# Optimization experiments

Measured on AMD Instinct MI355X. Metric: run time of the kernel, lower is better.

Reference implementation:

```python
import jax, jax.numpy as jnp
import numpy as np

LN_EPS = 1e-5
BN_EPS = 1e-5
N_TARGETS = 7


def setup_inputs() -> dict:
    key = jax.random.key(0)
    ks = jax.random.split(key, 12)
    B, N, W, Fin = 64, 40, 256, 64
    H, D = 4, 32
    C = H * D  # gat_out = 128
    L, K = 4, 3  # tcn layers / kernel
    FC = 128
    x = jax.random.normal(ks[0], (B, N, W, Fin), dtype=jnp.float32)
    adj = (jax.random.uniform(ks[1], (N, N)) < 0.3).astype(jnp.float32)
    adj = jnp.maximum(adj, jnp.eye(N, dtype=jnp.float32))  # self-loops
    s = 0.05
    return {
        "x": x,
        "adj": adj,
        "gat_w": jax.random.normal(ks[2], (C, Fin), dtype=jnp.float32) * s,
        "a_src": jax.random.normal(ks[3], (H, D), dtype=jnp.float32) * s,
        "a_dst": jax.random.normal(ks[4], (H, D), dtype=jnp.float32) * s,
        "ln_g": jnp.ones((C,), jnp.float32),
        "ln_b": jnp.zeros((C,), jnp.float32),
        "c1w": jax.random.normal(ks[5], (L, C, C, K), dtype=jnp.float32) * s,
        "c1b": jnp.zeros((L, C), jnp.float32),
        "c2w": jax.random.normal(ks[6], (L, C, C, K), dtype=jnp.float32) * s,
        "c2b": jnp.zeros((L, C), jnp.float32),
        "bn1s": jnp.ones((L, C), jnp.float32),
        "bn1b": jnp.zeros((L, C), jnp.float32),
        "bn1m": jnp.zeros((L, C), jnp.float32),
        "bn1v": jnp.ones((L, C), jnp.float32),
        "bn2s": jnp.ones((L, C), jnp.float32),
        "bn2b": jnp.zeros((L, C), jnp.float32),
        "bn2m": jnp.zeros((L, C), jnp.float32),
        "bn2v": jnp.ones((L, C), jnp.float32),
        "f1w": jax.random.normal(ks[7], (FC, C), dtype=jnp.float32) * s,
        "f1b": jnp.zeros((FC,), jnp.float32),
        "f2w": jax.random.normal(ks[8], (1, FC), dtype=jnp.float32) * s,
        "f2b": jnp.zeros((1,), jnp.float32),
    }


def reference(x, adj, gat_w, a_src, a_dst, ln_g, ln_b,
              c1w, c1b, c2w, c2b,
              bn1s, bn1b, bn1m, bn1v, bn2s, bn2b, bn2m, bn2v,
              f1w, f1b, f2w, f2b):
    B, N, W, Fin = x.shape
    H, D = a_src.shape
    C = H * D
    # --- GAT, vectorized over all W timesteps at once (same math as the per-t loop) ---
    h = jnp.einsum('bnwf,of->bnwo', x, gat_w).reshape(B, N, W, H, D)
    e_src = jnp.einsum('bnwhd,hd->bnwh', h, a_src)  # (B,N,W,H)
    e_dst = jnp.einsum('bnwhd,hd->bnwh', h, a_dst)
    # scores[b,i,w,h,j] = leaky_relu(e_src[b,i] + e_dst[b,j])
    scores = e_src[:, :, :, :, None] + jnp.transpose(e_dst, (0, 2, 3, 1))[:, None]  # (B,N,W,H,N)
    scores = jax.nn.leaky_relu(scores, 0.2)
    mask = adj[None, :, None, None, :] != 0
    scores = jnp.where(mask, scores, -1e9)
    attn = jax.nn.softmax(scores, axis=-1)  # softmax over destination j
    gat = jnp.einsum('bnwhj,bjwhd->bnwhd', attn, h).reshape(B, N, W, C)
    # --- LayerNorm over feature dim ---
    mu = gat.mean(-1, keepdims=True)
    var = gat.var(-1, keepdims=True)
    g = (gat - mu) / jnp.sqrt(var + LN_EPS) * ln_g + ln_b
    # --- TCN over per-node temporal sequences: (B*N, C, W) ---
    seq = jnp.transpose(g.reshape(B * N, W, C), (0, 2, 1))
    K = c1w.shape[-1]

    def bn(z, s, b, m, v):
        return (z - m[None, :, None]) / jnp.sqrt(v[None, :, None] + BN_EPS) * s[None, :, None] + b[None, :, None]

    def cconv(z, w, b, dil):
        pad = (K - 1) * dil  # causal left-padding
        y = jax.lax.conv_general_dilated(z, w, window_strides=(1,), padding=[(pad, 0)],
                                         rhs_dilation=(dil,), dimension_numbers=('NCH', 'OIH', 'NCH'))
        return y + b[None, :, None]

    cur = seq
    for i in range(c1w.shape[0]):  # fixed small number of TCN blocks
        dil = 2 ** i
        o = jax.nn.gelu(bn(cconv(cur, c1w[i], c1b[i], dil), bn1s[i], bn1b[i], bn1m[i], bn1v[i]), approximate=False)
        o = jax.nn.gelu(bn(cconv(o, c2w[i], c2b[i], dil), bn2s[i], bn2b[i], bn2m[i], bn2v[i]), approximate=False)
        cur = jax.nn.gelu(o + cur, approximate=False)  # residual is Identity (in_ch == out_ch)
    h_last = cur[:, :, -1].reshape(B, N, C)
    t = h_last[:, :N_TARGETS, :]  # target_indices = range(7)
    z = jax.nn.gelu(jnp.einsum('bnc,hc->bnh', t, f1w) + f1b, approximate=False)
    logits = (jnp.einsum('bnh,oh->bno', z, f2w) + f2b)[..., 0]  # (B, 7)
    return logits
```

## Files before the change

kernel.cpp:

```cpp
#include <hip/hip_runtime.h>
#include <hip/hip_bf16.h>
#include <math.h>

#define Bb   64
#define Nn   40
#define Ww   256
#define FIN  64
#define Hh   4
#define Dd   32
#define Cc   128
#define NT   7
#define FC   128
#define WT   61
#define W0   195
#define PSTRIDE 520
#define HS   132

#define SEQHI_OFF  0u
#define SEQ_BYTES  (448u * WT * Cc * 2u)
#define SEQLO_OFF  (SEQHI_OFF + SEQ_BYTES)
#define WBH_OFF    (SEQLO_OFF + SEQ_BYTES)
#define WB_BYTES   (8u * 4u * 24u * 64u * 8u * 2u)
#define WBL_OFF    (WBH_OFF + WB_BYTES)
#define PSB_OFF    (WBL_OFF + WB_BYTES)
#define PSS_OFF    (PSB_OFF + 4096u)
#define PSH_OFF    (PSS_OFF + 4096u)
#define WGH_OFF    (PSH_OFF + 4096u)
#define WGL_OFF    (WGH_OFF + 16384u)
#define WPHASE_US  49152u

typedef __attribute__((ext_vector_type(8)))  short short8;
typedef __attribute__((ext_vector_type(16))) float f32x16;

__device__ __forceinline__ float gelu_exact(float v) {
    return 0.5f * v * (1.0f + erff(v * 0.70710678118654752440f));
}
__device__ __forceinline__ float b2f(ushort u) {
    union { uint i; float f; } c; c.i = ((uint)u) << 16; return c.f;
}
__device__ __forceinline__ void split_bf16(float v, ushort& h, ushort& l) {
    __hip_bfloat16 bh = __float2bfloat16(v);
    float fh = __bfloat162float(bh);
    __hip_bfloat16 bl = __float2bfloat16(v - fh);
    h = *(ushort*)&bh; l = *(ushort*)&bl;
}

__global__ __launch_bounds__(256) void prep_kernel(
    const float* __restrict__ c1w, const float* __restrict__ c1b,
    const float* __restrict__ c2w, const float* __restrict__ c2b,
    const float* __restrict__ bn1s, const float* __restrict__ bn1b,
    const float* __restrict__ bn1m, const float* __restrict__ bn1v,
    const float* __restrict__ bn2s, const float* __restrict__ bn2b,
    const float* __restrict__ bn2m, const float* __restrict__ bn2v,
    const float* __restrict__ gat_w,
    char* __restrict__ ws)
{
    if (blockIdx.x < 192) {
        const int t = blockIdx.x * 256 + threadIdx.x;
        const int lane  = t & 63;
        const int kstep = (t >> 6) % 24;
        const int nt    = ((t >> 6) / 24) & 3;
        const int p     = (t >> 6) / 96;
        const int l = p >> 1, cv = p & 1;
        const int co = nt * 32 + (lane & 31);
        const float* wsrc = cv ? c2w : c1w;
        ushort* wbh = (ushort*)(ws + WBH_OFF);
        ushort* wbl = (ushort*)(ws + WBL_OFF);
#pragma unroll
        for (int j = 0; j < 8; ++j) {
            const int k  = kstep * 16 + ((lane >> 5) << 3) + j;
            const int kk = k >> 7, ci = k & 127;
            const float w = wsrc[((size_t)(l * Cc + co) * Cc + ci) * 3 + kk];
            ushort h, lo; split_bf16(w, h, lo);
            wbh[(size_t)t * 8 + j] = h;
            wbl[(size_t)t * 8 + j] = lo;
        }
    } else if (blockIdx.x == 192) {
        float* psb = (float*)(ws + PSB_OFF);
        float* pss = (float*)(ws + PSS_OFF);
        float* psh = (float*)(ws + PSH_OFF);
        for (int idx = threadIdx.x; idx < 1024; idx += 256) {
            const int p = idx >> 7, co = idx & 127;
            const int l = p >> 1, cv = p & 1;
            const int lc = l * Cc + co;
            const float s  = cv ? bn2s[lc] : bn1s[lc];
            const float bb = cv ? bn2b[lc] : bn1b[lc];
            const float m  = cv ? bn2m[lc] : bn1m[lc];
            const float vv = cv ? bn2v[lc] : bn1v[lc];
            const float cb = cv ? c2b[lc] : c1b[lc];
            const float scale = s * rsqrtf(vv + 1e-5f);
            pss[idx] = scale;
            psh[idx] = bb - m * scale;
            psb[idx] = cb;
        }
    } else {
        ushort* wgh = (ushort*)(ws + WGH_OFF);
        ushort* wgl = (ushort*)(ws + WGL_OFF);
#pragma unroll
        for (int it = 0; it < 4; ++it) {
            const int t = it * 256 + threadIdx.x;
            const int lane = t & 63;
            const int ks   = (t >> 6) & 3;
            const int nt   = t >> 8;
            const int co   = nt * 32 + (lane & 31);
#pragma unroll
            for (int j = 0; j < 8; ++j) {
                const int k = ks * 16 + ((lane >> 5) << 3) + j;
                ushort h, lo; split_bf16(gat_w[co * FIN + k], h, lo);
                wgh[t * 8 + j] = h;
                wgl[t * 8 + j] = lo;
            }
        }
    }
}

__global__ __launch_bounds__(256) void gat_ln_kernel(
    const float* __restrict__ x, const float* __restrict__ adj,
    const char* __restrict__ ws_ro,
    const float* __restrict__ a_src, const float* __restrict__ a_dst,
    const float* __restrict__ ln_g, const float* __restrict__ ln_b,
    ushort* __restrict__ seq_hi, ushort* __restrict__ seq_lo)
{
    __shared__ __align__(16) ushort xa_hi[8 * PSTRIDE];
    __shared__ __align__(16) ushort xa_lo[8 * PSTRIDE];
    __shared__ __align__(16) float h_lds[Nn * HS];
    __shared__ __align__(16) float e_lds[2 * Nn * Hh];
    __shared__ __align__(16) float attn_lds[NT * Hh * Nn];
    __shared__ __align__(16) float g_lds[NT * Cc];

    const int tid = threadIdx.x;
    const int blk = blockIdx.x;
    const int b   = blk / WT;
    const int tau = blk % WT;
    const int w   = W0 + tau;

    for (int idx = tid; idx < Nn * 8; idx += 256) {
        const int n  = idx >> 3;
        const int oc = idx & 7;
        const float* src = x + ((size_t)(b * Nn + n) * Ww + w) * FIN + oc * 8;
        const float4 f0 = *(const float4*)(src);
        const float4 f1 = *(const float4*)(src + 4);
        ushort h[8], l[8];
        split_bf16(f0.x, h[0], l[0]); split_bf16(f0.y, h[1], l[1]);
        split_bf16(f0.z, h[2], l[2]); split_bf16(f0.w, h[3], l[3]);
        split_bf16(f1.x, h[4], l[4]); split_bf16(f1.y, h[5], l[5]);
        split_bf16(f1.z, h[6], l[6]); split_bf16(f1.w, h[7], l[7]);
        const int dst = oc * PSTRIDE + n * 8;
        *(uint4*)(xa_hi + dst) = *(uint4*)h;
        *(uint4*)(xa_lo + dst) = *(uint4*)l;
    }
    for (int idx = tid; idx < 8 * (64 - Nn); idx += 256) {
        const int oc = idx / (64 - Nn);
        const int n  = Nn + idx % (64 - Nn);
        const int dst = oc * PSTRIDE + n * 8;
        uint4 z; z.x = z.y = z.z = z.w = 0u;
        *(uint4*)(xa_hi + dst) = z;
        *(uint4*)(xa_lo + dst) = z;
    }
    __syncthreads();

    {
        const int wave = tid >> 6;
        const int lane = tid & 63;
        const int nt   = wave;
        const int q2   = lane >> 5;
        const int m32  = lane & 31;
        const ushort* WGH = (const ushort*)(ws_ro + WGH_OFF);
        const ushort* WGL = (const ushort*)(ws_ro + WGL_OFF);

        f32x16 acc0, acc1;
#pragma unroll
        for (int i = 0; i < 16; ++i) { acc0[i] = 0.f; acc1[i] = 0.f; }

#pragma unroll
        for (int ks = 0; ks < 4; ++ks) {
            const size_t wo = ((size_t)((nt * 4 + ks) * 64 + lane)) * 8;
            const short8 bh = *(const short8*)(WGH + wo);
            const short8 bl = *(const short8*)(WGL + wo);
            const int pan = (ks * 2 + q2) * PSTRIDE;
            const short8 ah0 = *(const short8*)(xa_hi + pan + m32 * 8);
            const short8 al0 = *(const short8*)(xa_lo + pan + m32 * 8);
            const short8 ah1 = *(const short8*)(xa_hi + pan + (32 + m32) * 8);
            const short8 al1 = *(const short8*)(xa_lo + pan + (32 + m32) * 8);
            acc0 = __builtin_amdgcn_mfma_f32_32x32x16_bf16(ah0, bh, acc0, 0, 0, 0);
            acc0 = __builtin_amdgcn_mfma_f32_32x32x16_bf16(al0, bh, acc0, 0, 0, 0);
            acc0 = __builtin_amdgcn_mfma_f32_32x32x16_bf16(ah0, bl, acc0, 0, 0, 0);
            acc1 = __builtin_amdgcn_mfma_f32_32x32x16_bf16(ah1, bh, acc1, 0, 0, 0);
            acc1 = __builtin_amdgcn_mfma_f32_32x32x16_bf16(al1, bh, acc1, 0, 0, 0);
            acc1 = __builtin_amdgcn_mfma_f32_32x32x16_bf16(ah1, bl, acc1, 0, 0, 0);
        }

        const int co = nt * 32 + m32;
#pragma unroll
        for (int reg = 0; reg < 16; ++reg) {
            const int n = (reg & 3) + 8 * (reg >> 2) + 4 * q2;
            h_lds[n * HS + co] = acc0[reg];
        }
#pragma unroll
        for (int reg = 0; reg < 4; ++reg) {
            const int n = 32 + reg + 4 * q2;
            if (n < Nn) h_lds[n * HS + co] = acc1[reg];
        }
    }
    __syncthreads();

    for (int u = tid; u < 2 * Nn * Hh; u += 256) {
        const int s  = u & 1;
        const int hh = (u >> 1) & 3;
        const int n  = u >> 3;
        const float* av = (s ? a_dst : a_src) + hh * Dd;
        const float* hp = h_lds + n * HS + hh * Dd;
        float acc = 0.f;
#pragma unroll
        for (int i = 0; i < 8; ++i) {
            const float4 hv = *(const float4*)(hp + i * 4);
            const float4 avv = *(const float4*)(av + i * 4);
            acc += hv.x * avv.x + hv.y * avv.y + hv.z * avv.z + hv.w * avv.w;
        }
        e_lds[s * (Nn * Hh) + n * Hh + hh] = acc;
    }
    __syncthreads();

    if (tid < NT * Hh) {
        const int n  = tid >> 2;
        const int hh = tid & 3;
        const float es = e_lds[n * Hh + hh];
        float sc[Nn];
        float mx = -1e30f;
#pragma unroll
        for (int j = 0; j < Nn; ++j) {
            float s = es + e_lds[Nn * Hh + j * Hh + hh];
            s = (s > 0.f) ? s : 0.2f * s;
            if (adj[n * Nn + j] == 0.0f) s = -1e9f;
            sc[j] = s;
            mx = fmaxf(mx, s);
        }
        float sum = 0.f;
#pragma unroll
        for (int j = 0; j < Nn; ++j) { const float p = expf(sc[j] - mx); sc[j] = p; sum += p; }
        const float inv = 1.0f / sum;
#pragma unroll
        for (int j = 0; j < Nn; ++j)
            attn_lds[(n * Hh + hh) * Nn + j] = sc[j] * inv;
    }
    __syncthreads();

    if (tid < NT * 32) {
        const int n    = tid >> 5;
        const int cq   = tid & 31;
        const int c0   = cq * 4;
        const int head = cq >> 3;
        const float* ap = attn_lds + (n * Hh + head) * Nn;
        float4 acc = make_float4(0.f, 0.f, 0.f, 0.f);
        for (int j = 0; j < Nn; ++j) {
            const float a = ap[j];
            const float4 hv = *(const float4*)(h_lds + j * HS + c0);
            acc.x += a * hv.x; acc.y += a * hv.y;
            acc.z += a * hv.z; acc.w += a * hv.w;
        }
        *(float4*)(g_lds + n * Cc + c0) = acc;
    }
    __syncthreads();

    if (tid < NT * 32) {
        const int n = tid >> 5, lane = tid & 31;
        const float4 v = ((const float4*)(g_lds + n * Cc))[lane];
        float s  = v.x + v.y + v.z + v.w;
        float sq = v.x*v.x + v.y*v.y + v.z*v.z + v.w*v.w;
#pragma unroll
        for (int off = 16; off; off >>= 1) {
            s  += __shfl_xor(s, off, 32);
            sq += __shfl_xor(sq, off, 32);
        }
        const float mu   = s * (1.0f / Cc);
        const float rstd = rsqrtf(sq * (1.0f / Cc) - mu * mu + 1e-5f);
        const float4 gg = ((const float4*)ln_g)[lane];
        const float4 bb = ((const float4*)ln_b)[lane];
        float o0 = (v.x - mu) * rstd * gg.x + bb.x;
        float o1 = (v.y - mu) * rstd * gg.y + bb.y;
        float o2 = (v.z - mu) * rstd * gg.z + bb.z;
        float o3 = (v.w - mu) * rstd * gg.w + bb.w;
        const int r = b * NT + n;
        ushort4 uh, ul;
        split_bf16(o0, uh.x, ul.x);
        split_bf16(o1, uh.y, ul.y);
        split_bf16(o2, uh.z, ul.z);
        split_bf16(o3, uh.w, ul.w);
        const int p  = (lane >> 2) * 2 + ((lane >> 1) & 1);
        const int j0 = (lane & 1) * 4;
        const size_t off = ((size_t)(r * 16 + p) * WT + tau) * 8 + j0;
        *(ushort4*)(seq_hi + off) = uh;
        *(ushort4*)(seq_lo + off) = ul;
    }
}

__device__ __forceinline__ void conv_mfma(
    const ushort* in_hi, const ushort* in_lo,
    ushort* out_hi, ushort* out_lo,
    const ushort* __restrict__ wbh, const ushort* __restrict__ wbl,
    const float* __restrict__ psb, const float* __restrict__ pss,
    const float* __restrict__ psh,
    const int tau0, const int d, const int mt, const int nt,
    const int lane, const bool residual)
{
    const int m  = lane & 31;
    const int q2 = lane >> 5;
    const int co = nt * 32 + m;
    const int mbase = mt * 32 + m;

    const float bsv = psb[co], scv = pss[co], shv = psh[co];
    const int colb = ((co >> 4) * 2 + ((co >> 3) & 1)) * PSTRIDE + (co & 7);

    int rA0 = mbase - 2 * d; rA0 = rA0 < 0 ? 0 : rA0;
    int rA1 = mbase - d;     rA1 = rA1 < 0 ? 0 : rA1;
    const int rA2 = mbase;

    const ushort* wb_h = wbh + (size_t)(nt * 24) * 512 + lane * 8;
    const ushort* wb_l = wbl + (size_t)(nt * 24) * 512 + lane * 8;

    f32x16 acc0, acc1;
#pragma unroll
    for (int i = 0; i < 16; ++i) { acc0[i] = 0.f; acc1[i] = 0.f; }

    short8 WH[4], WL[4];
#pragma unroll
    for (int i = 0; i < 4; ++i) {
        WH[i] = *(const short8*)(wb_h + i * 512);
        WL[i] = *(const short8*)(wb_l + i * 512);
    }

#pragma unroll
    for (int ks = 0; ks < 24; ++ks) {
        const int slot = ks & 3;
        const short8 bh = WH[slot];
        const short8 bl = WL[slot];
        if (ks + 4 < 24) {
            WH[slot] = *(const short8*)(wb_h + (ks + 4) * 512);
            WL[slot] = *(const short8*)(wb_l + (ks + 4) * 512);
        }
        const int kk   = ks >> 3;
        const int rowA = (kk == 0) ? rA0 : (kk == 1 ? rA1 : rA2);
        const int aoff = (((ks & 7) << 1) + q2) * PSTRIDE + rowA * 8;
        const short8 ah = *(const short8*)(in_hi + aoff);
        const short8 al = *(const short8*)(in_lo + aoff);
        acc0 = __builtin_amdgcn_mfma_f32_32x32x16_bf16(ah, bh, acc0, 0, 0, 0);
        acc1 = __builtin_amdgcn_mfma_f32_32x32x16_bf16(al, bh, acc1, 0, 0, 0);
        if (ks & 1)
            acc0 = __builtin_amdgcn_mfma_f32_32x32x16_bf16(ah, bl, acc0, 0, 0, 0);
        else
            acc1 = __builtin_amdgcn_mfma_f32_32x32x16_bf16(ah, bl, acc1, 0, 0, 0);
    }
#pragma unroll
    for (int i = 0; i < 16; ++i) acc0[i] += acc1[i];

    float rc[16];
    if (residual) {
#pragma unroll
        for (int reg = 0; reg < 16; ++reg) {
            const int row = (reg & 3) + 8 * (reg >> 2) + 4 * q2;
            const int tau = mt * 32 + row;
            const int off = colb + tau * 8;
            rc[reg] = (tau >= tau0 && tau <= 60)
                    ? (b2f(out_hi[off]) + b2f(out_lo[off])) : 0.f;
        }
    }

#pragma unroll
    for (int reg = 0; reg < 16; ++reg) {
        const int row = (reg & 3) + 8 * (reg >> 2) + 4 * q2;
        const int tau = mt * 32 + row;
        if (tau >= tau0 && tau <= 60) {
            float v = (acc0[reg] + bsv) * scv + shv;
            v = gelu_exact(v);
            if (residual) v = gelu_exact(v + rc[reg]);
            ushort uh, ul; split_bf16(v, uh, ul);
            const int off = colb + tau * 8;
            out_hi[off] = uh; out_lo[off] = ul;
        }
    }
}

__global__ __launch_bounds__(512, 4) void tcn_head_kernel(
    const char* __restrict__ ws,
    const float* __restrict__ f1w, const float* __restrict__ f1b,
    const float* __restrict__ f2w, const float* __restrict__ f2b,
    float* __restrict__ out)
{
    __shared__ __align__(16) ushort cur_hi[16 * PSTRIDE];
    __shared__ __align__(16) ushort cur_lo[16 * PSTRIDE];
    __shared__ __align__(16) ushort o1_hi [16 * PSTRIDE];
    __shared__ __align__(16) ushort o1_lo [16 * PSTRIDE];
    __shared__ float red[FC];

    const int tid = threadIdx.x;
    const int r   = blockIdx.x;

    const ushort* seq_hi = (const ushort*)(ws + SEQHI_OFF);
    const ushort* seq_lo = (const ushort*)(ws + SEQLO_OFF);
    const ushort* WBH    = (const ushort*)(ws + WBH_OFF);
    const ushort* WBL    = (const ushort*)(ws + WBL_OFF);
    const float*  PSB    = (const float*)(ws + PSB_OFF);
    const float*  PSS    = (const float*)(ws + PSS_OFF);
    const float*  PSH    = (const float*)(ws + PSH_OFF);

    {
        const size_t base = (size_t)r * (16 * WT * 8);
        for (int i = tid; i < 16 * WT; i += 512) {
            const int p = i / WT, row = i - p * WT;
            const int dst = p * PSTRIDE + row * 8;
            *(uint4*)(cur_hi + dst) = *(const uint4*)(seq_hi + base + i * 8);
            *(uint4*)(cur_lo + dst) = *(const uint4*)(seq_lo + base + i * 8);
        }
    }
    __syncthreads();

    const int wave = tid >> 6;
    const int lane = tid & 63;
    const int nt   = wave & 3;
    const int mt   = wave >> 2;

    const int tau0_1[4] = {2, 8, 20, 44};
    const int tau0_2[4] = {4, 12, 28, 60};

#pragma unroll
    for (int l = 0; l < 4; ++l) {
        const int d  = 1 << l;
        const int p1 = 2 * l, p2 = 2 * l + 1;
        conv_mfma(cur_hi, cur_lo, o1_hi, o1_lo,
                  WBH + (size_t)p1 * WPHASE_US, WBL + (size_t)p1 * WPHASE_US,
                  PSB + p1 * Cc, PSS + p1 * Cc, PSH + p1 * Cc,
                  tau0_1[l], d, mt, nt, lane, false);
        __syncthreads();
        conv_mfma(o1_hi, o1_lo, cur_hi, cur_lo,
                  WBH + (size_t)p2 * WPHASE_US, WBL + (size_t)p2 * WPHASE_US,
                  PSB + p2 * Cc, PSS + p2 * Cc, PSH + p2 * Cc,
                  tau0_2[l], d, mt, nt, lane, true);
        __syncthreads();
    }

    if (tid < FC) {
        const float4* wr = (const float4*)(f1w + tid * Cc);
        float acc = 0.f;
#pragma unroll
        for (int i = 0; i < Cc / 4; ++i) {
            const float4 wv = wr[i];
            const int ci0 = i * 4;
            const int off = ((ci0 >> 4) * 2 + ((ci0 >> 3) & 1)) * PSTRIDE
                          + 60 * 8 + (ci0 & 7);
            acc += wv.x * (b2f(cur_hi[off + 0]) + b2f(cur_lo[off + 0]))
                 + wv.y * (b2f(cur_hi[off + 1]) + b2f(cur_lo[off + 1]))
                 + wv.z * (b2f(cur_hi[off + 2]) + b2f(cur_lo[off + 2]))
                 + wv.w * (b2f(cur_hi[off + 3]) + b2f(cur_lo[off + 3]));
        }
        red[tid] = gelu_exact(acc + f1b[tid]) * f2w[tid];
    }
    __syncthreads();
    if (tid < 64) {
        float v = red[tid] + red[tid + 64];
#pragma unroll
        for (int off = 32; off; off >>= 1) v += __shfl_xor(v, off, 64);
        if (tid == 0) out[r] = v + f2b[0];
    }
}

extern "C" void kernel_launch(void* const* d_in, const int* in_sizes, int n_in,
                              void* d_out, int out_size, void* d_ws, size_t ws_size,
                              hipStream_t stream) {
    const float* x     = (const float*)d_in[0];
    const float* adj   = (const float*)d_in[1];
    const float* gat_w = (const float*)d_in[2];
    const float* a_src = (const float*)d_in[3];
    const float* a_dst = (const float*)d_in[4];
    const float* ln_g  = (const float*)d_in[5];
    const float* ln_b  = (const float*)d_in[6];
    const float* c1w   = (const float*)d_in[7];
    const float* c1b   = (const float*)d_in[8];
    const float* c2w   = (const float*)d_in[9];
    const float* c2b   = (const float*)d_in[10];
    const float* bn1s  = (const float*)d_in[11];
    const float* bn1b  = (const float*)d_in[12];
    const float* bn1m  = (const float*)d_in[13];
    const float* bn1v  = (const float*)d_in[14];
    const float* bn2s  = (const float*)d_in[15];
    const float* bn2b  = (const float*)d_in[16];
    const float* bn2m  = (const float*)d_in[17];
    const float* bn2v  = (const float*)d_in[18];
    const float* f1w   = (const float*)d_in[19];
    const float* f1b   = (const float*)d_in[20];
    const float* f2w   = (const float*)d_in[21];
    const float* f2b   = (const float*)d_in[22];

    char* ws = (char*)d_ws;

    prep_kernel<<<194, 256, 0, stream>>>(c1w, c1b, c2w, c2b,
        bn1s, bn1b, bn1m, bn1v, bn2s, bn2b, bn2m, bn2v, gat_w, ws);

    gat_ln_kernel<<<Bb * WT, 256, 0, stream>>>(
        x, adj, ws, a_src, a_dst, ln_g, ln_b,
        (ushort*)(ws + SEQHI_OFF), (ushort*)(ws + SEQLO_OFF));

    tcn_head_kernel<<<Bb * NT, 512, 0, stream>>>(
        ws, f1w, f1b, f2w, f2b, (float*)d_out);
}
```

Measured before the change: 387.3 us.

## Process two timesteps per GAT block and skip dead TCN row tiles

Each GAT/LayerNorm block now handles two consecutive timesteps. The 80 node rows are packed into three 32-row MFMA tiles, so the GAT weight fragments are loaded into registers once and reused across both timesteps, which halves the grid size and reduces padding waste. In the TCN, conv_mfma returns early for row tiles that lie entirely before the receptive-field start tau0, and the head kernel reads its hi/lo activations with vector loads. The shared-memory buffers are aliased into one pool to limit LDS use, at the cost of more bookkeeping for the odd final timestep group.

```diff
diff --git a/kernel.cpp b/kernel.cpp
--- a/kernel.cpp
+++ b/kernel.cpp
@@ -14,7 +14,12 @@
 #define WT   61
 #define W0   195
 #define PSTRIDE 520
-#define HS   132
+#define HS2  132
+
+#define GTAUS 2
+#define NTG   31
+#define XPAN  768
+#define GROWS 80
 
 #define SEQHI_OFF  0u
 #define SEQ_BYTES  (448u * WT * Cc * 2u)
@@ -121,41 +126,40 @@
     const float* __restrict__ ln_g, const float* __restrict__ ln_b,
     ushort* __restrict__ seq_hi, ushort* __restrict__ seq_lo)
 {
-    __shared__ __align__(16) ushort xa_hi[8 * PSTRIDE];
-    __shared__ __align__(16) ushort xa_lo[8 * PSTRIDE];
-    __shared__ __align__(16) float h_lds[Nn * HS];
-    __shared__ __align__(16) float e_lds[2 * Nn * Hh];
-    __shared__ __align__(16) float attn_lds[NT * Hh * Nn];
-    __shared__ __align__(16) float g_lds[NT * Cc];
+    __shared__ __align__(16) char pool[2 * 12288];
+    __shared__ __align__(16) float h_lds[GROWS * HS2];
+
+    ushort* xa_hi = (ushort*)pool;
+    ushort* xa_lo = (ushort*)(pool + 12288);
+    float* e_lds    = (float*)pool;
+    float* attn_lds = (float*)(pool + 2560);
+    float* g_lds    = (float*)(pool + 11520);
 
     const int tid = threadIdx.x;
-    const int blk = blockIdx.x;
-    const int b   = blk / WT;
-    const int tau = blk % WT;
-    const int w   = W0 + tau;
-
-    for (int idx = tid; idx < Nn * 8; idx += 256) {
-        const int n  = idx >> 3;
-        const int oc = idx & 7;
-        const float* src = x + ((size_t)(b * Nn + n) * Ww + w) * FIN + oc * 8;
-        const float4 f0 = *(const float4*)(src);
-        const float4 f1 = *(const float4*)(src + 4);
-        ushort h[8], l[8];
-        split_bf16(f0.x, h[0], l[0]); split_bf16(f0.y, h[1], l[1]);
-        split_bf16(f0.z, h[2], l[2]); split_bf16(f0.w, h[3], l[3]);
-        split_bf16(f1.x, h[4], l[4]); split_bf16(f1.y, h[5], l[5]);
-        split_bf16(f1.z, h[6], l[6]); split_bf16(f1.w, h[7], l[7]);
-        const int dst = oc * PSTRIDE + n * 8;
-        *(uint4*)(xa_hi + dst) = *(uint4*)h;
-        *(uint4*)(xa_lo + dst) = *(uint4*)l;
-    }
-    for (int idx = tid; idx < 8 * (64 - Nn); idx += 256) {
-        const int oc = idx / (64 - Nn);
-        const int n  = Nn + idx % (64 - Nn);
-        const int dst = oc * PSTRIDE + n * 8;
-        uint4 z; z.x = z.y = z.z = z.w = 0u;
-        *(uint4*)(xa_hi + dst) = z;
-        *(uint4*)(xa_lo + dst) = z;
+    const int b   = blockIdx.x / NTG;
+    const int tg  = blockIdx.x % NTG;
+    const int tau0g  = tg * GTAUS;
+    const int nvalid = (tau0g + 1 < WT) ? 2 : 1;
+
+    for (int idx = tid; idx < GTAUS * Nn * 8; idx += 256) {
+        const int tl  = idx >= 320;
+        const int rem = idx - tl * 320;
+        const int n  = rem >> 3;
+        const int oc = rem & 7;
+        if (tl < nvalid) {
+            const int w = W0 + tau0g + tl;
+            const float* src = x + ((size_t)(b * Nn + n) * Ww + w) * FIN + oc * 8;
+            const float4 f0 = *(const float4*)(src);
+            const float4 f1 = *(const float4*)(src + 4);
+            ushort h[8], l[8];
+            split_bf16(f0.x, h[0], l[0]); split_bf16(f0.y, h[1], l[1]);
+            split_bf16(f0.z, h[2], l[2]); split_bf16(f0.w, h[3], l[3]);
+            split_bf16(f1.x, h[4], l[4]); split_bf16(f1.y, h[5], l[5]);
+            split_bf16(f1.z, h[6], l[6]); split_bf16(f1.w, h[7], l[7]);
+            const int dst = oc * XPAN + (tl * Nn + n) * 8;
+            *(uint4*)(xa_hi + dst) = *(uint4*)h;
+            *(uint4*)(xa_lo + dst) = *(uint4*)l;
+        }
     }
     __syncthreads();
 
@@ -168,48 +172,46 @@
         const ushort* WGH = (const ushort*)(ws_ro + WGH_OFF);
         const ushort* WGL = (const ushort*)(ws_ro + WGL_OFF);
 
-        f32x16 acc0, acc1;
-#pragma unroll
-        for (int i = 0; i < 16; ++i) { acc0[i] = 0.f; acc1[i] = 0.f; }
-
+        short8 BH[4], BL[4];
 #pragma unroll
         for (int ks = 0; ks < 4; ++ks) {
             const size_t wo = ((size_t)((nt * 4 + ks) * 64 + lane)) * 8;
-            const short8 bh = *(const short8*)(WGH + wo);
-            const short8 bl = *(const short8*)(WGL + wo);
-            const int pan = (ks * 2 + q2) * PSTRIDE;
-            const short8 ah0 = *(const short8*)(xa_hi + pan + m32 * 8);
-            const short8 al0 = *(const short8*)(xa_lo + pan + m32 * 8);
-            const short8 ah1 = *(const short8*)(xa_hi + pan + (32 + m32) * 8);
-            const short8 al1 = *(const short8*)(xa_lo + pan + (32 + m32) * 8);
-            acc0 = __builtin_amdgcn_mfma_f32_32x32x16_bf16(ah0, bh, acc0, 0, 0, 0);
-            acc0 = __builtin_amdgcn_mfma_f32_32x32x16_bf16(al0, bh, acc0, 0, 0, 0);
-            acc0 = __builtin_amdgcn_mfma_f32_32x32x16_bf16(ah0, bl, acc0, 0, 0, 0);
-            acc1 = __builtin_amdgcn_mfma_f32_32x32x16_bf16(ah1, bh, acc1, 0, 0, 0);
-            acc1 = __builtin_amdgcn_mfma_f32_32x32x16_bf16(al1, bh, acc1, 0, 0, 0);
-            acc1 = __builtin_amdgcn_mfma_f32_32x32x16_bf16(ah1, bl, acc1, 0, 0, 0);
-        }
-
+            BH[ks] = *(const short8*)(WGH + wo);
+            BL[ks] = *(const short8*)(WGL + wo);
+        }
         const int co = nt * 32 + m32;
-#pragma unroll
-        for (int reg = 0; reg < 16; ++reg) {
-            const int n = (reg & 3) + 8 * (reg >> 2) + 4 * q2;
-            h_lds[n * HS + co] = acc0[reg];
-        }
-#pragma unroll
-        for (int reg = 0; reg < 4; ++reg) {
-            const int n = 32 + reg + 4 * q2;
-            if (n < Nn) h_lds[n * HS + co] = acc1[reg];
-        }
-    }
-    __syncthreads();
-
-    for (int u = tid; u < 2 * Nn * Hh; u += 256) {
-        const int s  = u & 1;
-        const int hh = (u >> 1) & 3;
-        const int n  = u >> 3;
+
+#pragma unroll
+        for (int mt = 0; mt < 3; ++mt) {
+            f32x16 acc;
+#pragma unroll
+            for (int i = 0; i < 16; ++i) acc[i] = 0.f;
+#pragma unroll
+            for (int ks = 0; ks < 4; ++ks) {
+                const int aoff = (ks * 2 + q2) * XPAN + (mt * 32 + m32) * 8;
+                const short8 ah = *(const short8*)(xa_hi + aoff);
+                const short8 al = *(const short8*)(xa_lo + aoff);
+                acc = __builtin_amdgcn_mfma_f32_32x32x16_bf16(ah, BH[ks], acc, 0, 0, 0);
+                acc = __builtin_amdgcn_mfma_f32_32x32x16_bf16(al, BH[ks], acc, 0, 0, 0);
+                acc = __builtin_amdgcn_mfma_f32_32x32x16_bf16(ah, BL[ks], acc, 0, 0, 0);
+            }
+#pragma unroll
+            for (int reg = 0; reg < 16; ++reg) {
+                const int row = mt * 32 + (reg & 3) + 8 * (reg >> 2) + 4 * q2;
+                if (row < GROWS) h_lds[row * HS2 + co] = acc[reg];
+            }
+        }
+    }
+    __syncthreads();
+
+    for (int u = tid; u < GTAUS * 2 * Nn * Hh; u += 256) {
+        const int tl = u >= 320;
+        const int uu = u - tl * 320;
+        const int s  = uu & 1;
+        const int hh = (uu >> 1) & 3;
+        const int n  = uu >> 3;
         const float* av = (s ? a_dst : a_src) + hh * Dd;
-        const float* hp = h_lds + n * HS + hh * Dd;
+        const float* hp = h_lds + (tl * Nn + n) * HS2 + hh * Dd;
         float acc = 0.f;
 #pragma unroll
         for (int i = 0; i < 8; ++i) {
@@ -217,80 +219,94 @@
             const float4 avv = *(const float4*)(av + i * 4);
             acc += hv.x * avv.x + hv.y * avv.y + hv.z * avv.z + hv.w * avv.w;
         }
-        e_lds[s * (Nn * Hh) + n * Hh + hh] = acc;
-    }
-    __syncthreads();
-
-    if (tid < NT * Hh) {
-        const int n  = tid >> 2;
-        const int hh = tid & 3;
-        const float es = e_lds[n * Hh + hh];
-        float sc[Nn];
-        float mx = -1e30f;
-#pragma unroll
-        for (int j = 0; j < Nn; ++j) {
-            float s = es + e_lds[Nn * Hh + j * Hh + hh];
-            s = (s > 0.f) ? s : 0.2f * s;
-            if (adj[n * Nn + j] == 0.0f) s = -1e9f;
-            sc[j] = s;
-            mx = fmaxf(mx, s);
-        }
-        float sum = 0.f;
-#pragma unroll
-        for (int j = 0; j < Nn; ++j) { const float p = expf(sc[j] - mx); sc[j] = p; sum += p; }
-        const float inv = 1.0f / sum;
-#pragma unroll
-        for (int j = 0; j < Nn; ++j)
-            attn_lds[(n * Hh + hh) * Nn + j] = sc[j] * inv;
-    }
-    __syncthreads();
-
-    if (tid < NT * 32) {
-        const int n    = tid >> 5;
-        const int cq   = tid & 31;
+        e_lds[((tl * 2 + s) * Nn + n) * Hh + hh] = acc;
+    }
+    __syncthreads();
+
+    if (tid < GTAUS * NT * Hh) {
+        const int tl = tid >= NT * Hh;
+        const int i  = tid - tl * NT * Hh;
+        const int n  = i >> 2;
+        const int hh = i & 3;
+        if (tl < nvalid) {
+            const float es = e_lds[((tl * 2 + 0) * Nn + n) * Hh + hh];
+            float sc[Nn];
+            float mx = -1e30f;
+#pragma unroll
+            for (int j = 0; j < Nn; ++j) {
+                float s = es + e_lds[((tl * 2 + 1) * Nn + j) * Hh + hh];
+                s = (s > 0.f) ? s : 0.2f * s;
+                if (adj[n * Nn + j] == 0.0f) s = -1e9f;
+                sc[j] = s;
+                mx = fmaxf(mx, s);
+            }
+            float sum = 0.f;
+#pragma unroll
+            for (int j = 0; j < Nn; ++j) { const float p = expf(sc[j] - mx); sc[j] = p; sum += p; }
+            const float inv = 1.0f / sum;
+#pragma unroll
+            for (int j = 0; j < Nn; ++j)
+                attn_lds[((tl * NT + n) * Hh + hh) * Nn + j] = sc[j] * inv;
+        }
+    }
+    __syncthreads();
+
+    for (int u = tid; u < GTAUS * NT * 32; u += 256) {
+        const int tl = u >= NT * 32;
+        const int i  = u - tl * NT * 32;
+        const int n    = i >> 5;
+        const int cq   = i & 31;
         const int c0   = cq * 4;
         const int head = cq >> 3;
-        const float* ap = attn_lds + (n * Hh + head) * Nn;
-        float4 acc = make_float4(0.f, 0.f, 0.f, 0.f);
-        for (int j = 0; j < Nn; ++j) {
-            const float a = ap[j];
-            const float4 hv = *(const float4*)(h_lds + j * HS + c0);
-            acc.x += a * hv.x; acc.y += a * hv.y;
-            acc.z += a * hv.z; acc.w += a * hv.w;
-        }
-        *(float4*)(g_lds + n * Cc + c0) = acc;
-    }
-    __syncthreads();
-
-    if (tid < NT * 32) {
-        const int n = tid >> 5, lane = tid & 31;
-        const float4 v = ((const float4*)(g_lds + n * Cc))[lane];
-        float s  = v.x + v.y + v.z + v.w;
-        float sq = v.x*v.x + v.y*v.y + v.z*v.z + v.w*v.w;
-#pragma unroll
-        for (int off = 16; off; off >>= 1) {
-            s  += __shfl_xor(s, off, 32);
-            sq += __shfl_xor(sq, off, 32);
-        }
-        const float mu   = s * (1.0f / Cc);
-        const float rstd = rsqrtf(sq * (1.0f / Cc) - mu * mu + 1e-5f);
-        const float4 gg = ((const float4*)ln_g)[lane];
-        const float4 bb = ((const float4*)ln_b)[lane];
-        float o0 = (v.x - mu) * rstd * gg.x + bb.x;
-        float o1 = (v.y - mu) * rstd * gg.y + bb.y;
-        float o2 = (v.z - mu) * rstd * gg.z + bb.z;
-        float o3 = (v.w - mu) * rstd * gg.w + bb.w;
-        const int r = b * NT + n;
-        ushort4 uh, ul;
-        split_bf16(o0, uh.x, ul.x);
-        split_bf16(o1, uh.y, ul.y);
-        split_bf16(o2, uh.z, ul.z);
-        split_bf16(o3, uh.w, ul.w);
-        const int p  = (lane >> 2) * 2 + ((lane >> 1) & 1);
-        const int j0 = (lane & 1) * 4;
-        const size_t off = ((size_t)(r * 16 + p) * WT + tau) * 8 + j0;
-        *(ushort4*)(seq_hi + off) = uh;
-        *(ushort4*)(seq_lo + off) = ul;
+        if (tl < nvalid) {
+            const float* ap = attn_lds + ((tl * NT + n) * Hh + head) * Nn;
+            float4 acc = make_float4(0.f, 0.f, 0.f, 0.f);
+            for (int j = 0; j < Nn; ++j) {
+                const float a = ap[j];
+                const float4 hv = *(const float4*)(h_lds + (tl * Nn + j) * HS2 + c0);
+                acc.x += a * hv.x; acc.y += a * hv.y;
+                acc.z += a * hv.z; acc.w += a * hv.w;
+            }
+            *(float4*)(g_lds + (tl * NT + n) * Cc + c0) = acc;
+        }
+    }
+    __syncthreads();
+
+    for (int u = tid; u < GTAUS * NT * 32; u += 256) {
+        const int tl = u >= NT * 32;
+        const int i  = u - tl * NT * 32;
+        const int n  = i >> 5;
+        const int lane = u & 31;
+        if (tl < nvalid) {
+            const float4 v = ((const float4*)(g_lds + (tl * NT + n) * Cc))[lane];
+            float s  = v.x + v.y + v.z + v.w;
+            float sq = v.x*v.x + v.y*v.y + v.z*v.z + v.w*v.w;
+#pragma unroll
+            for (int off = 16; off; off >>= 1) {
+                s  += __shfl_xor(s, off, 32);
+                sq += __shfl_xor(sq, off, 32);
+            }
+            const float mu   = s * (1.0f / Cc);
+            const float rstd = rsqrtf(sq * (1.0f / Cc) - mu * mu + 1e-5f);
+            const float4 gg = ((const float4*)ln_g)[lane];
+            const float4 bb = ((const float4*)ln_b)[lane];
+            float o0 = (v.x - mu) * rstd * gg.x + bb.x;
+            float o1 = (v.y - mu) * rstd * gg.y + bb.y;
+            float o2 = (v.z - mu) * rstd * gg.z + bb.z;
+            float o3 = (v.w - mu) * rstd * gg.w + bb.w;
+            const int r = b * NT + n;
+            const int tau = tau0g + tl;
+            ushort4 uh, ul;
+            split_bf16(o0, uh.x, ul.x);
+            split_bf16(o1, uh.y, ul.y);
+            split_bf16(o2, uh.z, ul.z);
+            split_bf16(o3, uh.w, ul.w);
+            const int p  = (lane >> 2) * 2 + ((lane >> 1) & 1);
+            const int j0 = (lane & 1) * 4;
+            const size_t off = ((size_t)(r * 16 + p) * WT + tau) * 8 + j0;
+            *(ushort4*)(seq_hi + off) = uh;
+            *(ushort4*)(seq_lo + off) = ul;
+        }
     }
 }
 
@@ -303,6 +319,8 @@
     const int tau0, const int d, const int mt, const int nt,
     const int lane, const bool residual)
 {
+    if (mt * 32 + 31 < tau0) return;
+
     const int m  = lane & 31;
     const int q2 = lane >> 5;
     const int co = nt * 32 + m;
@@ -447,10 +465,12 @@
             const int ci0 = i * 4;
             const int off = ((ci0 >> 4) * 2 + ((ci0 >> 3) & 1)) * PSTRIDE
                           + 60 * 8 + (ci0 & 7);
-            acc += wv.x * (b2f(cur_hi[off + 0]) + b2f(cur_lo[off + 0]))
-                 + wv.y * (b2f(cur_hi[off + 1]) + b2f(cur_lo[off + 1]))
-                 + wv.z * (b2f(cur_hi[off + 2]) + b2f(cur_lo[off + 2]))
-                 + wv.w * (b2f(cur_hi[off + 3]) + b2f(cur_lo[off + 3]));
+            const ushort4 vh = *(const ushort4*)(cur_hi + off);
+            const ushort4 vl = *(const ushort4*)(cur_lo + off);
+            acc += wv.x * (b2f(vh.x) + b2f(vl.x))
+                 + wv.y * (b2f(vh.y) + b2f(vl.y))
+                 + wv.z * (b2f(vh.z) + b2f(vl.z))
+                 + wv.w * (b2f(vh.w) + b2f(vl.w));
         }
         red[tid] = gelu_exact(acc + f1b[tid]) * f2w[tid];
     }
@@ -495,7 +515,7 @@
     prep_kernel<<<194, 256, 0, stream>>>(c1w, c1b, c2w, c2b,
         bn1s, bn1b, bn1m, bn1v, bn2s, bn2b, bn2m, bn2v, gat_w, ws);
 
-    gat_ln_kernel<<<Bb * WT, 256, 0, stream>>>(
+    gat_ln_kernel<<<Bb * NTG, 256, 0, stream>>>(
         x, adj, ws, a_src, a_dst, ln_g, ln_b,
         (ushort*)(ws + SEQHI_OFF), (ushort*)(ws + SEQLO_OFF));
 
```

Measured after the change: 384.2 us. No clear change (-0.8%).
